# Optimization experiments

Hardware: AMD Instinct MI355X
Metric: run time of the kernel (lower is better)

Reference implementation:

```python
import jax, jax.numpy as jnp
import numpy as np

V, D, N, M, H, W, K = 97, 512, 128, 64, 8, 8, 3
HALF = K // 2
DH = D // H
RPL = M + 3 + K   # key(M) + beta + gate + shift(K) + gamma = 70
WPL = RPL + 2 * M # + erase(M) + add(M) = 198
B, T = 32, 128


def _ln(x, g, b):
    mu = x.mean(-1, keepdims=True)
    var = ((x - mu) ** 2).mean(-1, keepdims=True)
    return (x - mu) / jnp.sqrt(var + 1e-5) * g + b


def _addressing(key, beta, gate, shift, gamma, prev_w, memory):
    # key [B,M], beta/gate/gamma [B,1], shift [B,K], prev_w [B,N], memory [B,N,M]
    eps = 1e-12
    kn = key / (jnp.linalg.norm(key, axis=-1, keepdims=True) + eps)
    mn = memory / (jnp.linalg.norm(memory, axis=-1, keepdims=True) + eps)
    cos = jnp.einsum('bnm,bm->bn', mn, kn)
    wc = jax.nn.softmax(jax.nn.softplus(beta) * cos, axis=-1)
    g = jax.nn.sigmoid(gate)
    wg = g * wc + (1.0 - g) * prev_w
    s = jax.nn.softmax(shift, axis=-1)
    shifted = sum(s[:, k:k + 1] * jnp.roll(wg, k - HALF, axis=-1) for k in range(K))
    gp = 1.0 + jax.nn.softplus(gamma)
    wt = (shifted + eps) ** gp
    return wt / (wt.sum(-1, keepdims=True) + eps)


def setup_inputs() -> dict:
    key = jax.random.key(0)
    ks = jax.random.split(key, 16)
    s = 0.05
    return {
        'x': jax.random.randint(ks[0], (B, T), 0, V),
        'emb': jax.random.normal(ks[1], (V, D)) * 0.02,
        'W_in': jax.random.normal(ks[2], (D, D + M)) * s,
        'b_in': jnp.zeros((D,)),
        'W_qkv': jax.random.normal(ks[3], (3 * D, D)) * s,
        'b_qkv': jnp.zeros((3 * D,)),
        'W_o': jax.random.normal(ks[4], (D, D)) * s,
        'b_o': jnp.zeros((D,)),
        'ln1_g': jnp.ones((D,)), 'ln1_b': jnp.zeros((D,)),
        'W_ff1': jax.random.normal(ks[5], (4 * D, D)) * s,
        'b_ff1': jnp.zeros((4 * D,)),
        'W_ff2': jax.random.normal(ks[6], (D, 4 * D)) * s,
        'b_ff2': jnp.zeros((D,)),
        'ln2_g': jnp.ones((D,)), 'ln2_b': jnp.zeros((D,)),
        'W_tok': jax.random.normal(ks[7], (V, D)) * s,
        'b_tok': jnp.zeros((V,)),
        'W_read': jax.random.normal(ks[8], (RPL, D)) * s,
        'b_read': jnp.zeros((RPL,)),
        'W_write': jax.random.normal(ks[9], (WPL, D)) * s,
        'b_write': jnp.zeros((WPL,)),
    }


def _forward(x, emb, W_in, b_in, W_qkv, b_qkv, W_o, b_o, ln1_g, ln1_b,
             W_ff1, b_ff1, W_ff2, b_ff2, ln2_g, ln2_b, W_tok, b_tok,
             W_read, b_read, W_write, b_write):
    Wq, Wk, Wv = W_qkv[:D], W_qkv[D:2 * D], W_qkv[2 * D:]
    bq, bk, bv = b_qkv[:D], b_qkv[D:2 * D], b_qkv[2 * D:]
    scale = 1.0 / np.sqrt(DH)

    def step(carry, x_t):
        memory, rw, ww, cache, t = carry
        tok = emb[x_t]                                   # [B,D]
        r = jnp.einsum('bn,bnm->bm', rw, memory)         # read vector [B,M]
        wide = jnp.concatenate([tok, r], -1)             # [B,D+M]
        xp = wide @ W_in.T + b_in                        # [B,D]
        q = xp[None]                                     # [1,B,D]
        # kv buffer: cache (detached) + current q, truncated to last W
        kbuf = jnp.concatenate([cache, q], 0)[-W:]       # [W,B,D]
        valid = jnp.arange(W) >= W - jnp.minimum(t + 1, W)
        qh = (xp @ Wq.T + bq).reshape(-1, H, DH)         # [B,H,DH]
        kh = (kbuf @ Wk.T + bk).reshape(W, -1, H, DH)    # [W,B,H,DH]
        vh = (kbuf @ Wv.T + bv).reshape(W, -1, H, DH)
        scores = jnp.einsum('bhe,wbhe->bhw', qh, kh) * scale
        scores = jnp.where(valid[None, None, :], scores, -jnp.inf)
        attn = jax.nn.softmax(scores, axis=-1)
        ctx = jnp.einsum('bhw,wbhe->bhe', attn, vh).reshape(-1, D)
        attn_out = ctx @ W_o.T + b_o
        x2 = _ln(xp + attn_out, ln1_g, ln1_b)
        ff = jax.nn.gelu(x2 @ W_ff1.T + b_ff1, approximate=False) @ W_ff2.T + b_ff2
        out = _ln(x2 + ff, ln2_g, ln2_b)
        logits = out @ W_tok.T + b_tok
        # read head addressing (RH=1)
        rp = out @ W_read.T + b_read
        new_rw = _addressing(rp[:, :M], rp[:, M:M + 1], rp[:, M + 1:M + 2],
                             rp[:, M + 2:M + 2 + K], rp[:, M + 2 + K:M + 3 + K],
                             rw, memory)
        # write head addressing + erase/add (WH=1)
        wp = out @ W_write.T + b_write
        new_ww = _addressing(wp[:, :M], wp[:, M:M + 1], wp[:, M + 1:M + 2],
                             wp[:, M + 2:M + 2 + K], wp[:, M + 2 + K:M + 3 + K],
                             ww, memory)
        erase = jax.nn.sigmoid(wp[:, RPL:RPL + M])       # [B,M]
        add = jnp.tanh(wp[:, RPL + M:])                  # [B,M]
        new_mem = memory * (1.0 - new_ww[:, :, None] * erase[:, None, :]) \
                  + new_ww[:, :, None] * add[:, None, :]
        new_cache = jax.lax.stop_gradient(jnp.concatenate([cache, q], 0)[-W:])
        return (new_mem, new_rw, new_ww, new_cache, t + 1), logits

    Bv = x.shape[0]
    mem0 = jnp.zeros((Bv, N, M), jnp.float32)
    w0 = jnp.zeros((Bv, N), jnp.float32).at[:, 0].set(1.0)
    cache0 = jnp.zeros((W, Bv, D), jnp.float32)
    carry0 = (mem0, w0, w0, cache0, jnp.int32(0))
    _, logits = jax.lax.scan(step, carry0, x.T)          # [T,B,V]
    return jnp.transpose(logits, (1, 0, 2))              # [B,T,V]


def reference(x, emb, W_in, b_in, W_qkv, b_qkv, W_o, b_o, ln1_g, ln1_b,
              W_ff1, b_ff1, W_ff2, b_ff2, ln2_g, ln2_b, W_tok, b_tok,
              W_read, b_read, W_write, b_write):
    return _forward(x, emb, W_in, b_in, W_qkv, b_qkv, W_o, b_o, ln1_g, ln1_b,
                    W_ff1, b_ff1, W_ff2, b_ff2, ln2_g, ln2_b, W_tok, b_tok,
                    W_read, b_read, W_write, b_write)
```

## Files before the change

kernel.cpp:

```cpp
#include <hip/hip_runtime.h>
#include <math.h>

static constexpr int Tc = 128, Vc = 97;

static constexpr size_t T_FQ  = 0;
static constexpr size_t BF    = T_FQ + (size_t)576*1536;
static constexpr size_t T_IN  = BF + 1536;
static constexpr size_t T_O   = T_IN + (size_t)576*512;
static constexpr size_t T_FF1 = T_O + (size_t)512*512;
static constexpr size_t T_FF2 = T_FF1 + (size_t)512*2048;
static constexpr size_t T_TOK = T_FF2 + (size_t)2048*512;
static constexpr size_t T_RW  = T_TOK + (size_t)512*128;
static constexpr size_t ARENA = T_RW + (size_t)512*288;
static constexpr size_t TEAM_STRIDE = 8704;
static constexpr size_t A_YP = 0;
static constexpr size_t A_OP = 4096;
static constexpr size_t A_RWP = 8192;
static constexpr size_t FLG = ARENA + (size_t)32*TEAM_STRIDE;

__device__ __forceinline__ float softplusf_(float x) { return x > 20.f ? x : log1pf(expf(x)); }
__device__ __forceinline__ float sigmoidf_(float x) { return 1.f / (1.f + expf(-x)); }

__device__ __forceinline__ float wsum(float v) {
#pragma unroll
  for (int o = 1; o < 64; o <<= 1) v += __shfl_xor(v, o);
  return v;
}
__device__ __forceinline__ float wmax(float v) {
#pragma unroll
  for (int o = 1; o < 64; o <<= 1) v = fmaxf(v, __shfl_xor(v, o));
  return v;
}

__device__ __forceinline__ void st_llc(float* p, float v) {
  __hip_atomic_store(p, v, __ATOMIC_RELAXED, __HIP_MEMORY_SCOPE_SYSTEM);
}
__device__ __forceinline__ float ld_llc(const float* p) {
  return __hip_atomic_load(p, __ATOMIC_RELAXED, __HIP_MEMORY_SCOPE_SYSTEM);
}
__device__ __forceinline__ void st_flag(int* p, int v) {
  __hip_atomic_store(p, v, __ATOMIC_RELAXED, __HIP_MEMORY_SCOPE_SYSTEM);
}
__device__ __forceinline__ int ld_flag(const int* p) {
  return __hip_atomic_load(p, __ATOMIC_RELAXED, __HIP_MEMORY_SCOPE_SYSTEM);
}

#define PUBF(stage)                                                      \
  do {                                                                   \
    asm volatile("s_waitcnt vmcnt(0)" ::: "memory");                     \
    __syncthreads();                                                     \
    if (tid == 0) st_flag(flg + (stage)*128 + sq*16, t + 1);             \
  } while (0)

#define WAITF(stage, need)                                               \
  do {                                                                   \
    if (tid < 8) {                                                       \
      while (ld_flag(flg + (stage)*128 + tid*16) < (need))               \
        __builtin_amdgcn_s_sleep(1);                                     \
    }                                                                    \
    __syncthreads();                                                     \
    asm volatile("" ::: "memory");                                       \
  } while (0)

template <int NCH, int CH, int NG, int SF4>
__device__ __forceinline__ void mvp(const float* __restrict__ wbase,
                                    const float* __restrict__ src,
                                    float* part, int tid) {
  const int cs = tid / NG, g = tid % NG;
  const float4* __restrict__ w4 =
      reinterpret_cast<const float4*>(wbase + (size_t)cs * CH * (SF4 * 4)) + g;
  const float* __restrict__ v = src + cs * CH;
  float a0 = 0.f, a1 = 0.f, a2 = 0.f, a3 = 0.f;
#pragma unroll 8
  for (int c = 0; c < CH; ++c) {
    float4 w = w4[(size_t)c * SF4];
    float vv = v[c];
    a0 += vv * w.x; a1 += vv * w.y; a2 += vv * w.z; a3 += vv * w.w;
  }
  *reinterpret_cast<float4*>(part + tid * 4) = make_float4(a0, a1, a2, a3);
}

__global__ __launch_bounds__(256) void k_init(const float* __restrict__ W_in,
                                              const float* __restrict__ W_qkv,
                                              const float* __restrict__ W_o,
                                              const float* __restrict__ W_ff1,
                                              const float* __restrict__ W_ff2,
                                              const float* __restrict__ W_tok,
                                              const float* __restrict__ W_read,
                                              const float* __restrict__ W_write,
                                              const float* __restrict__ b_qkv,
                                              const float* __restrict__ b_in,
                                              float* __restrict__ ws) {
  const size_t tid = (size_t)blockIdx.x * 256 + threadIdx.x;
  const size_t nth = (size_t)gridDim.x * 256;
  for (size_t i = tid; i < (size_t)576*512; i += nth) {
    size_t c = i >> 9, j = i & 511;
    ws[T_IN + i] = W_in[j * 576 + c];
  }
  for (size_t i = tid; i < (size_t)512*512; i += nth) {
    size_t e = i >> 9, j = i & 511;
    ws[T_O + i] = W_o[j * 512 + e];
  }
  for (size_t i = tid; i < (size_t)512*2048; i += nth) {
    size_t d = i >> 11, f = i & 2047;
    ws[T_FF1 + i] = W_ff1[f * 512 + d];
  }
  for (size_t i = tid; i < (size_t)2048*512; i += nth) {
    size_t k = i >> 9, j = i & 511;
    ws[T_FF2 + i] = W_ff2[j * 2048 + k];
  }
  for (size_t i = tid; i < (size_t)512*128; i += nth) {
    size_t d = i >> 7, j = i & 127;
    int qq = (int)(j >> 4), i2 = (int)(j & 15);
    int v = qq * 13 + i2;
    ws[T_TOK + i] = (i2 < 13 && v < 97) ? W_tok[(size_t)v * 512 + d] : 0.f;
  }
  for (size_t i = tid; i < (size_t)512*288; i += nth) {
    size_t d = i / 288, j = i % 288;
    int qq = (int)(j / 36), i2 = (int)(j % 36);
    int idx = qq * 34 + i2;
    float val = 0.f;
    if (i2 < 34 && idx < 268)
      val = (idx < 70) ? W_read[(size_t)idx * 512 + d] : W_write[(size_t)(idx - 70) * 512 + d];
    ws[T_RW + i] = val;
  }
  for (size_t j = tid; j < 1536; j += nth) {
    float a = b_qkv[j];
    const float* r = W_qkv + j * 512;
    for (int d = 0; d < 512; ++d) a += r[d] * b_in[d];
    ws[BF + j] = a;
  }
  for (size_t i = tid; i < (size_t)32 * TEAM_STRIDE; i += nth) ws[ARENA + i] = 0.f;
  for (size_t i = tid; i < 32768; i += nth) ((int*)(ws + FLG))[i] = 0;
}

__global__ __launch_bounds__(256) void k_fuse(const float* __restrict__ W_qkv,
                                              const float* __restrict__ W_in,
                                              float* __restrict__ ws) {
  __shared__ float As[32][64];
  __shared__ float Bs[32][96];
  const int cb = blockIdx.x % 9, jb = blockIdx.x / 9;
  const int c0 = cb * 64, j0 = jb * 96;
  const int tid = threadIdx.x;
  float acc[24];
#pragma unroll
  for (int u = 0; u < 24; ++u) acc[u] = 0.f;
  for (int d0 = 0; d0 < 512; d0 += 32) {
    __syncthreads();
    for (int i = tid; i < 32 * 64; i += 256) { int dd = i >> 6, cc = i & 63; As[dd][cc] = W_in[(size_t)(d0 + dd) * 576 + c0 + cc]; }
    for (int i = tid; i < 32 * 96; i += 256) { int jj = i >> 5, dd = i & 31; Bs[dd][jj] = W_qkv[(size_t)(j0 + jj) * 512 + d0 + dd]; }
    __syncthreads();
    const int tc = tid & 63, jbase = (tid >> 6) * 24;
    for (int dd = 0; dd < 32; ++dd) {
      float a = As[dd][tc];
#pragma unroll
      for (int u = 0; u < 24; ++u) acc[u] += a * Bs[dd][jbase + u];
    }
  }
  const int tc = tid & 63, jbase = (tid >> 6) * 24;
#pragma unroll
  for (int u = 0; u < 24; ++u)
    ws[T_FQ + (size_t)(c0 + tc) * 1536 + j0 + jbase + u] = acc[u];
}

__global__ __launch_bounds__(512) void k_main(
    const int* __restrict__ x, const float* __restrict__ emb,
    const float* __restrict__ b_in, const float* __restrict__ b_o,
    const float* __restrict__ ln1g, const float* __restrict__ ln1b,
    const float* __restrict__ b_ff1, const float* __restrict__ b_ff2,
    const float* __restrict__ ln2g, const float* __restrict__ ln2b,
    const float* __restrict__ b_tok,
    const float* __restrict__ b_read, const float* __restrict__ b_write,
    float* __restrict__ ws, float* __restrict__ dout) {
  const float* __restrict__ wt = ws;
  const int wg = blockIdx.x, tid = threadIdx.x;
  const int sq = wg & 7, b = wg >> 3;
  const int wv = tid >> 6, ln = tid & 63;
  float* ar = ws + ARENA + (size_t)b * TEAM_STRIDE;
  int* flg = (int*)(ws + FLG) + b * 1024;

  __shared__ float memS[128 * 64];
  __shared__ float kcS[8 * 64], vcS[8 * 64];
  __shared__ float rwvS[128], wwvS[128], wwnS[128];
  __shared__ float rvec[64];
  __shared__ float wideS[576];
  __shared__ float xpSl[64];
  __shared__ float qhS[64];
  __shared__ float scoresS[8], awS[8];
  __shared__ float ctxH[64];
  __shared__ float yS[512], x2S[512], oS[512], onS[512];
  __shared__ float hSl[256];
  __shared__ __align__(16) float part[2048];
  __shared__ float rwpS[272];
  __shared__ float cosS[256];
  __shared__ float redA[8], redB[8];
  __shared__ float eS[64], aS[64];

  for (int i = tid; i < 8192; i += 512) memS[i] = 0.f;
  if (tid < 128) { float v0 = (tid == 0) ? 1.f : 0.f; rwvS[tid] = v0; wwvS[tid] = v0; }
  __syncthreads();

  for (int t = 0; t < Tc; ++t) {
    {
      float a = 0.f;
#pragma unroll
      for (int k2 = 0; k2 < 16; ++k2) { int n = wv * 16 + k2; a += rwvS[n] * memS[n * 64 + ln]; }
      part[wv * 64 + ln] = a;
    }
    __syncthreads();
    if (tid < 64) {
      float s = 0.f;
#pragma unroll
      for (int p = 0; p < 8; ++p) s += part[p * 64 + tid];
      rvec[tid] = s;
    }
    __syncthreads();
    const int tok = x[b * Tc + t];
    for (int i = tid; i < 576; i += 512)
      wideS[i] = (i < 512) ? emb[(size_t)tok * 512 + i] : rvec[i - 512];
    __syncthreads();

    const int slot = t & 7;
    for (int p3 = 0; p3 < 3; ++p3) {
      mvp<32, 18, 16, 384>(wt + T_FQ + p3 * 512 + 64 * sq, wideS, part, tid);
      __syncthreads();
      if (tid < 64) {
        float s = wt[BF + p3 * 512 + 64 * sq + tid];
#pragma unroll
        for (int cs = 0; cs < 32; ++cs) s += part[cs * 64 + tid];
        if (p3 == 0) qhS[tid] = s;
        else if (p3 == 1) kcS[slot * 64 + tid] = s;
        else vcS[slot * 64 + tid] = s;
      }
      __syncthreads();
    }
    mvp<32, 18, 16, 128>(wt + T_IN + 64 * sq, wideS, part, tid);
    __syncthreads();
    if (tid < 64) {
      float s = b_in[64 * sq + tid];
#pragma unroll
      for (int cs = 0; cs < 32; ++cs) s += part[cs * 64 + tid];
      xpSl[tid] = s;
    }
    __syncthreads();

    {
      int st = t - 7 + wv;
      float c = 0.f;
      if (st >= 0) c = qhS[ln] * kcS[(st & 7) * 64 + ln];
      c = wsum(c);
      if (ln == 0) scoresS[wv] = (st >= 0) ? c * 0.125f : -INFINITY;
    }
    __syncthreads();
    if (tid == 0) {
      float mx = -INFINITY;
      for (int j = 0; j < 8; ++j) mx = fmaxf(mx, scoresS[j]);
      float e[8], ssum = 0.f;
      for (int j = 0; j < 8; ++j) { e[j] = expf(scoresS[j] - mx); ssum += e[j]; }
      float inv = 1.f / ssum;
      for (int j = 0; j < 8; ++j) awS[j] = e[j] * inv;
    }
    __syncthreads();
    if (tid < 64) {
      float a = 0.f;
#pragma unroll
      for (int j = 0; j < 8; ++j) {
        int st = t - 7 + j;
        if (st >= 0) a += awS[j] * vcS[(st & 7) * 64 + tid];
      }
      ctxH[tid] = a;
    }
    __syncthreads();

    mvp<4, 16, 128, 128>(wt + T_O + (size_t)64 * sq * 512, ctxH, part, tid);
    __syncthreads();
    {
      float s = 0.f;
#pragma unroll
      for (int cs = 0; cs < 4; ++cs) s += part[cs * 512 + tid];
      if ((tid >> 6) == sq) s += xpSl[tid & 63];
      st_llc(ar + A_YP + sq * 512 + tid, s);
    }
    PUBF(0);
    WAITF(0, t + 1);
    {
      float s = b_o[tid];
#pragma unroll
      for (int q2 = 0; q2 < 8; ++q2) s += ld_llc(ar + A_YP + q2 * 512 + tid);
      yS[tid] = s;
    }
    __syncthreads();
    {
      float v = yS[tid];
      float a = wsum(v), b2 = wsum(v * v);
      if (ln == 0) { redA[wv] = a; redB[wv] = b2; }
      __syncthreads();
      float sa = 0.f, sb = 0.f;
#pragma unroll
      for (int i2 = 0; i2 < 8; ++i2) { sa += redA[i2]; sb += redB[i2]; }
      float mu = sa * (1.f / 512.f);
      float var = sb * (1.f / 512.f) - mu * mu;
      float rstd = rsqrtf(var + 1e-5f);
      x2S[tid] = (yS[tid] - mu) * rstd * ln1g[tid] + ln1b[tid];
    }
    __syncthreads();

    mvp<8, 64, 64, 512>(wt + T_FF1 + 256 * sq, x2S, part, tid);
    __syncthreads();
    if (tid < 256) {
      float s = b_ff1[256 * sq + tid];
#pragma unroll
      for (int cs = 0; cs < 8; ++cs) s += part[cs * 256 + tid];
      hSl[tid] = 0.5f * s * (1.f + erff(s * 0.70710678118654752f));
    }
    __syncthreads();

    mvp<4, 64, 128, 128>(wt + T_FF2 + (size_t)256 * sq * 512, hSl, part, tid);
    __syncthreads();
    {
      float s = 0.f;
#pragma unroll
      for (int cs = 0; cs < 4; ++cs) s += part[cs * 512 + tid];
      st_llc(ar + A_OP + sq * 512 + tid, s);
    }
    PUBF(1);
    WAITF(1, t + 1);
    {
      float s = b_ff2[tid] + x2S[tid];
#pragma unroll
      for (int q2 = 0; q2 < 8; ++q2) s += ld_llc(ar + A_OP + q2 * 512 + tid);
      oS[tid] = s;
    }
    __syncthreads();
    {
      float v = oS[tid];
      float a = wsum(v), b2 = wsum(v * v);
      if (ln == 0) { redA[wv] = a; redB[wv] = b2; }
      __syncthreads();
      float sa = 0.f, sb = 0.f;
#pragma unroll
      for (int i2 = 0; i2 < 8; ++i2) { sa += redA[i2]; sb += redB[i2]; }
      float mu = sa * (1.f / 512.f);
      float var = sb * (1.f / 512.f) - mu * mu;
      float rstd = rsqrtf(var + 1e-5f);
      onS[tid] = (oS[tid] - mu) * rstd * ln2g[tid] + ln2b[tid];
    }
    __syncthreads();

    if (tid < 288) {
      const int cs = tid / 9, g = tid % 9;
      const float4* __restrict__ w4 =
          reinterpret_cast<const float4*>(wt + T_RW + (size_t)(cs * 16) * 288 + 36 * sq) + g;
      const float* __restrict__ v = onS + cs * 16;
      float a0 = 0.f, a1 = 0.f, a2 = 0.f, a3 = 0.f;
#pragma unroll
      for (int c = 0; c < 16; ++c) {
        float4 w = w4[(size_t)c * 72];
        float vv = v[c];
        a0 += vv * w.x; a1 += vv * w.y; a2 += vv * w.z; a3 += vv * w.w;
      }
      *reinterpret_cast<float4*>(part + cs * 36 + g * 4) = make_float4(a0, a1, a2, a3);
    }
    __syncthreads();
    if (tid < 34) {
      int idx = 34 * sq + tid;
      if (idx < 268) {
        float s = (idx < 70) ? b_read[idx] : b_write[idx - 70];
#pragma unroll
        for (int cs = 0; cs < 32; ++cs) s += part[cs * 36 + tid];
        st_llc(ar + A_RWP + idx, s);
      }
    }
    PUBF(2);
    if (tid < 128) {
      const int cs = tid >> 2, g = tid & 3;
      const float4* __restrict__ w4 =
          reinterpret_cast<const float4*>(wt + T_TOK + (size_t)(cs * 16) * 128 + 16 * sq) + g;
      const float* __restrict__ v = onS + cs * 16;
      float a0 = 0.f, a1 = 0.f, a2 = 0.f, a3 = 0.f;
#pragma unroll
      for (int c = 0; c < 16; ++c) {
        float4 w = w4[(size_t)c * 32];
        float vv = v[c];
        a0 += vv * w.x; a1 += vv * w.y; a2 += vv * w.z; a3 += vv * w.w;
      }
      *reinterpret_cast<float4*>(part + tid * 4) = make_float4(a0, a1, a2, a3);
    }
    __syncthreads();
    if (tid < 13) {
      int v = 13 * sq + tid;
      if (v < Vc) {
        float s = b_tok[v];
#pragma unroll
        for (int cs = 0; cs < 32; ++cs) s += part[cs * 16 + tid];
        dout[((size_t)b * Tc + t) * Vc + v] = s;
      }
    }
    WAITF(2, t + 1);
    if (tid < 268) rwpS[tid] = ld_llc(ar + A_RWP + tid);
    __syncthreads();

    for (int p = 0; p < 32; ++p) {
      int idx = wv * 32 + p;
      int ksel = idx >> 7, row = idx & 127;
      const float* key = ksel ? (rwpS + 70) : rwpS;
      float m = memS[row * 64 + ln];
      float pp = m * key[ln], qq = m * m;
#pragma unroll
      for (int o = 1; o < 64; o <<= 1) { pp += __shfl_xor(pp, o); qq += __shfl_xor(qq, o); }
      if (ln == 0) cosS[idx] = pp / (sqrtf(qq) + 1e-12f);
    }
    __syncthreads();
    if (wv < 2) {
      const float* P = wv ? (rwpS + 70) : rwpS;
      const float* cosb = cosS + wv * 128;
      float* prevw = wv ? wwvS : rwvS;
      float kk = P[ln];
      float kn2 = wsum(kk * kk);
      float kinv = 1.f / (sqrtf(kn2) + 1e-12f);
      float beta = softplusf_(P[64]);
      float g = sigmoidf_(P[65]);
      float sh0 = P[66], sh1 = P[67], sh2 = P[68];
      float m3 = fmaxf(sh0, fmaxf(sh1, sh2));
      float es0 = expf(sh0 - m3), es1 = expf(sh1 - m3), es2 = expf(sh2 - m3);
      float i3 = 1.f / (es0 + es1 + es2);
      es0 *= i3; es1 *= i3; es2 *= i3;
      float gp = 1.f + softplusf_(P[69]);
      float v0 = beta * cosb[ln] * kinv, v1 = beta * cosb[64 + ln] * kinv;
      float mx = wmax(fmaxf(v0, v1));
      float e0 = expf(v0 - mx), e1 = expf(v1 - mx);
      float einv = 1.f / wsum(e0 + e1);
      float w0 = g * e0 * einv + (1.f - g) * prevw[ln];
      float w1 = g * e1 * einv + (1.f - g) * prevw[64 + ln];
      float w0m = __shfl(w0, (ln + 63) & 63), w1m = __shfl(w1, (ln + 63) & 63);
      float w0p = __shfl(w0, (ln + 1) & 63),  w1p = __shfl(w1, (ln + 1) & 63);
      float prev0 = (ln == 0)  ? w1m : w0m;
      float next0 = (ln == 63) ? w1p : w0p;
      float prev1 = (ln == 0)  ? w0m : w1m;
      float next1 = (ln == 63) ? w0p : w1p;
      float t0 = es0 * next0 + es1 * w0 + es2 * prev0;
      float t1 = es0 * next1 + es1 * w1 + es2 * prev1;
      float wt0 = powf(t0 + 1e-12f, gp), wt1 = powf(t1 + 1e-12f, gp);
      float winv = 1.f / (wsum(wt0 + wt1) + 1e-12f);
      w0 = wt0 * winv; w1 = wt1 * winv;
      prevw[ln] = w0; prevw[64 + ln] = w1;
      if (wv) { wwnS[ln] = w0; wwnS[64 + ln] = w1; }
    } else if (wv == 2) {
      eS[ln] = sigmoidf_(rwpS[140 + ln]);
      aS[ln] = tanhf(rwpS[204 + ln]);
    }
    __syncthreads();
    for (int i = tid; i < 8192; i += 512) {
      int n = i >> 6, m = i & 63;
      float wn = wwnS[n];
      memS[i] = memS[i] * (1.f - wn * eS[m]) + wn * aS[m];
    }
    __syncthreads();
  }
}

extern "C" void kernel_launch(void* const* d_in, const int* in_sizes, int n_in,
                              void* d_out, int out_size, void* d_ws, size_t ws_size,
                              hipStream_t stream) {
  (void)in_sizes; (void)n_in; (void)out_size; (void)ws_size;
  const int* x = (const int*)d_in[0];
  const float* emb = (const float*)d_in[1];
  const float* W_in = (const float*)d_in[2];
  const float* b_in = (const float*)d_in[3];
  const float* W_qkv = (const float*)d_in[4];
  const float* b_qkv = (const float*)d_in[5];
  const float* W_o = (const float*)d_in[6];
  const float* b_o = (const float*)d_in[7];
  const float* ln1g = (const float*)d_in[8];
  const float* ln1b = (const float*)d_in[9];
  const float* W_ff1 = (const float*)d_in[10];
  const float* b_ff1 = (const float*)d_in[11];
  const float* W_ff2 = (const float*)d_in[12];
  const float* b_ff2 = (const float*)d_in[13];
  const float* ln2g = (const float*)d_in[14];
  const float* ln2b = (const float*)d_in[15];
  const float* W_tok = (const float*)d_in[16];
  const float* b_tok = (const float*)d_in[17];
  const float* W_read = (const float*)d_in[18];
  const float* b_read = (const float*)d_in[19];
  const float* W_write = (const float*)d_in[20];
  const float* b_write = (const float*)d_in[21];
  float* ws = (float*)d_ws;
  float* out = (float*)d_out;

  hipLaunchKernelGGL(k_init, dim3(512), dim3(256), 0, stream,
                     W_in, W_qkv, W_o, W_ff1, W_ff2, W_tok, W_read, W_write,
                     b_qkv, b_in, ws);
  hipLaunchKernelGGL(k_fuse, dim3(144), dim3(256), 0, stream, W_qkv, W_in, ws);
  hipLaunchKernelGGL(k_main, dim3(256), dim3(512), 0, stream,
                     x, emb, b_in, b_o, ln1g, ln1b, b_ff1, b_ff2,
                     ln2g, ln2b, b_tok, b_read, b_write, ws, out);
}
```

Before: 6.163 ms.

## Repartition persistent kernel by output columns across whole batch with global stage flags

The persistent kernel no longer has each batch row handled by a team of 8 workgroups. Each workgroup now computes a column slice of every projection (QKV/in, O, FF1, FF2, read/write, token logits) for all 32 batch rows, so each weight slice is loaded once into LDS and reused across the batch. Stages are chained through global flags and atomic stores. Memory addressing stays on 32 workgroups, which now also keep the memory row norms incrementally. The change trades heavy per-team weight streaming for more grid-wide synchronization points per timestep (about six global barriers per step).

```diff
diff --git a/kernel.cpp b/kernel.cpp
--- a/kernel.cpp
+++ b/kernel.cpp
@@ -3,20 +3,24 @@
 
 static constexpr int Tc = 128, Vc = 97;
 
-static constexpr size_t T_FQ  = 0;
-static constexpr size_t BF    = T_FQ + (size_t)576*1536;
-static constexpr size_t T_IN  = BF + 1536;
-static constexpr size_t T_O   = T_IN + (size_t)576*512;
-static constexpr size_t T_FF1 = T_O + (size_t)512*512;
-static constexpr size_t T_FF2 = T_FF1 + (size_t)512*2048;
-static constexpr size_t T_TOK = T_FF2 + (size_t)2048*512;
-static constexpr size_t T_RW  = T_TOK + (size_t)512*128;
-static constexpr size_t ARENA = T_RW + (size_t)512*288;
-static constexpr size_t TEAM_STRIDE = 8704;
-static constexpr size_t A_YP = 0;
-static constexpr size_t A_OP = 4096;
-static constexpr size_t A_RWP = 8192;
-static constexpr size_t FLG = ARENA + (size_t)32*TEAM_STRIDE;
+static constexpr size_t T_FQ = 0;
+static constexpr size_t BF   = T_FQ + (size_t)576*1536;
+static constexpr size_t T_IN = BF + 1536;
+static constexpr size_t T_O  = T_IN + (size_t)576*512;
+static constexpr size_t T_FF1= T_O + (size_t)512*512;
+static constexpr size_t T_FF2= T_FF1 + (size_t)512*2048;
+static constexpr size_t T_RW = T_FF2 + (size_t)2048*512;
+static constexpr size_t A_WIDE = T_RW + (size_t)512*272;
+static constexpr size_t A_QKVX = A_WIDE + (size_t)32*576;
+static constexpr size_t A_CTX  = A_QKVX + (size_t)4*32*512;
+static constexpr size_t A_Y    = A_CTX + (size_t)32*512;
+static constexpr size_t A_H    = A_Y + (size_t)32*512;
+static constexpr size_t A_OUT  = A_H + (size_t)32*2048;
+static constexpr size_t A_X2   = A_OUT + (size_t)32*512;
+static constexpr size_t A_RWP  = A_X2 + (size_t)32*512;
+static constexpr size_t FLGO   = A_RWP + (size_t)32*272;
+static constexpr int FA_S=0, FB_S=256, FC1_S=512, FC2_S=768, FD_S=1024, FE1_S=1280, FE2_S=1536;
+static constexpr int NFLG_INT = 1792 * 16;
 
 __device__ __forceinline__ float softplusf_(float x) { return x > 20.f ? x : log1pf(expf(x)); }
 __device__ __forceinline__ float sigmoidf_(float x) { return 1.f / (1.f + expf(-x)); }
@@ -35,61 +39,34 @@
 __device__ __forceinline__ void st_llc(float* p, float v) {
   __hip_atomic_store(p, v, __ATOMIC_RELAXED, __HIP_MEMORY_SCOPE_SYSTEM);
 }
-__device__ __forceinline__ float ld_llc(const float* p) {
-  return __hip_atomic_load(p, __ATOMIC_RELAXED, __HIP_MEMORY_SCOPE_SYSTEM);
-}
 __device__ __forceinline__ void st_flag(int* p, int v) {
   __hip_atomic_store(p, v, __ATOMIC_RELAXED, __HIP_MEMORY_SCOPE_SYSTEM);
 }
 __device__ __forceinline__ int ld_flag(const int* p) {
   return __hip_atomic_load(p, __ATOMIC_RELAXED, __HIP_MEMORY_SCOPE_SYSTEM);
 }
-
-#define PUBF(stage)                                                      \
-  do {                                                                   \
-    asm volatile("s_waitcnt vmcnt(0)" ::: "memory");                     \
-    __syncthreads();                                                     \
-    if (tid == 0) st_flag(flg + (stage)*128 + sq*16, t + 1);             \
+__device__ __forceinline__ void wait1(const int* flg, int slot, int need) {
+  while (ld_flag(flg + slot * 16) < need) __builtin_amdgcn_s_sleep(1);
+}
+#define FENCE_ACQ() __builtin_amdgcn_fence(__ATOMIC_ACQUIRE, "agent")
+#define PUBF(slot)                                            \
+  do {                                                        \
+    asm volatile("s_waitcnt vmcnt(0)" ::: "memory");          \
+    __syncthreads();                                          \
+    if (tid == 0) st_flag(flg + (slot) * 16, t + 1);          \
   } while (0)
 
-#define WAITF(stage, need)                                               \
-  do {                                                                   \
-    if (tid < 8) {                                                       \
-      while (ld_flag(flg + (stage)*128 + tid*16) < (need))               \
-        __builtin_amdgcn_s_sleep(1);                                     \
-    }                                                                    \
-    __syncthreads();                                                     \
-    asm volatile("" ::: "memory");                                       \
-  } while (0)
-
-template <int NCH, int CH, int NG, int SF4>
-__device__ __forceinline__ void mvp(const float* __restrict__ wbase,
-                                    const float* __restrict__ src,
-                                    float* part, int tid) {
-  const int cs = tid / NG, g = tid % NG;
-  const float4* __restrict__ w4 =
-      reinterpret_cast<const float4*>(wbase + (size_t)cs * CH * (SF4 * 4)) + g;
-  const float* __restrict__ v = src + cs * CH;
-  float a0 = 0.f, a1 = 0.f, a2 = 0.f, a3 = 0.f;
-#pragma unroll 8
-  for (int c = 0; c < CH; ++c) {
-    float4 w = w4[(size_t)c * SF4];
-    float vv = v[c];
-    a0 += vv * w.x; a1 += vv * w.y; a2 += vv * w.z; a3 += vv * w.w;
-  }
-  *reinterpret_cast<float4*>(part + tid * 4) = make_float4(a0, a1, a2, a3);
-}
-
 __global__ __launch_bounds__(256) void k_init(const float* __restrict__ W_in,
-                                              const float* __restrict__ W_qkv,
                                               const float* __restrict__ W_o,
                                               const float* __restrict__ W_ff1,
                                               const float* __restrict__ W_ff2,
-                                              const float* __restrict__ W_tok,
                                               const float* __restrict__ W_read,
                                               const float* __restrict__ W_write,
+                                              const float* __restrict__ W_qkv,
                                               const float* __restrict__ b_qkv,
                                               const float* __restrict__ b_in,
+                                              const float* __restrict__ emb,
+                                              const int* __restrict__ x,
                                               float* __restrict__ ws) {
   const size_t tid = (size_t)blockIdx.x * 256 + threadIdx.x;
   const size_t nth = (size_t)gridDim.x * 256;
@@ -109,20 +86,12 @@
     size_t k = i >> 9, j = i & 511;
     ws[T_FF2 + i] = W_ff2[j * 2048 + k];
   }
-  for (size_t i = tid; i < (size_t)512*128; i += nth) {
-    size_t d = i >> 7, j = i & 127;
-    int qq = (int)(j >> 4), i2 = (int)(j & 15);
-    int v = qq * 13 + i2;
-    ws[T_TOK + i] = (i2 < 13 && v < 97) ? W_tok[(size_t)v * 512 + d] : 0.f;
-  }
-  for (size_t i = tid; i < (size_t)512*288; i += nth) {
-    size_t d = i / 288, j = i % 288;
-    int qq = (int)(j / 36), i2 = (int)(j % 36);
-    int idx = qq * 34 + i2;
-    float val = 0.f;
-    if (i2 < 34 && idx < 268)
-      val = (idx < 70) ? W_read[(size_t)idx * 512 + d] : W_write[(size_t)(idx - 70) * 512 + d];
-    ws[T_RW + i] = val;
+  for (size_t i = tid; i < (size_t)512*272; i += nth) {
+    size_t d = i / 272, j = i % 272;
+    float v = 0.f;
+    if (j < 70) v = W_read[j * 512 + d];
+    else if (j < 268) v = W_write[(j - 70) * 512 + d];
+    ws[T_RW + i] = v;
   }
   for (size_t j = tid; j < 1536; j += nth) {
     float a = b_qkv[j];
@@ -130,8 +99,11 @@
     for (int d = 0; d < 512; ++d) a += r[d] * b_in[d];
     ws[BF + j] = a;
   }
-  for (size_t i = tid; i < (size_t)32 * TEAM_STRIDE; i += nth) ws[ARENA + i] = 0.f;
-  for (size_t i = tid; i < 32768; i += nth) ((int*)(ws + FLG))[i] = 0;
+  for (size_t i = tid; i < (size_t)32*576; i += nth) {
+    size_t b = i / 576, c = i % 576;
+    ws[A_WIDE + i] = (c < 512) ? emb[(size_t)x[b * 128] * 512 + c] : 0.f;
+  }
+  for (size_t i = tid; i < (size_t)NFLG_INT; i += nth) ((int*)(ws + FLGO))[i] = 0;
 }
 
 __global__ __launch_bounds__(256) void k_fuse(const float* __restrict__ W_qkv,
@@ -169,293 +141,405 @@
     const float* __restrict__ ln1g, const float* __restrict__ ln1b,
     const float* __restrict__ b_ff1, const float* __restrict__ b_ff2,
     const float* __restrict__ ln2g, const float* __restrict__ ln2b,
-    const float* __restrict__ b_tok,
+    const float* __restrict__ W_tok, const float* __restrict__ b_tok,
     const float* __restrict__ b_read, const float* __restrict__ b_write,
     float* __restrict__ ws, float* __restrict__ dout) {
   const float* __restrict__ wt = ws;
-  const int wg = blockIdx.x, tid = threadIdx.x;
-  const int sq = wg & 7, b = wg >> 3;
-  const int wv = tid >> 6, ln = tid & 63;
-  float* ar = ws + ARENA + (size_t)b * TEAM_STRIDE;
-  int* flg = (int*)(ws + FLG) + b * 1024;
+  const int g = blockIdx.x, tid = threadIdx.x;
+  const int b = tid >> 4, u = tid & 15;
+  const int ln = tid & 63, wv = tid >> 6;
+  int* flg = (int*)(ws + FLGO);
 
   __shared__ float memS[128 * 64];
+  __shared__ float ssq[128];
   __shared__ float kcS[8 * 64], vcS[8 * 64];
   __shared__ float rwvS[128], wwvS[128], wwnS[128];
-  __shared__ float rvec[64];
-  __shared__ float wideS[576];
-  __shared__ float xpSl[64];
-  __shared__ float qhS[64];
-  __shared__ float scoresS[8], awS[8];
-  __shared__ float ctxH[64];
-  __shared__ float yS[512], x2S[512], oS[512], onS[512];
-  __shared__ float hSl[256];
-  __shared__ __align__(16) float part[2048];
+  __shared__ float xbuf[32 * 512];
+  __shared__ float wS[4608];
+  __shared__ float pbuf[4096];
   __shared__ float rwpS[272];
-  __shared__ float cosS[256];
-  __shared__ float redA[8], redB[8];
+  __shared__ float cosR[128], cosW[128];
   __shared__ float eS[64], aS[64];
-
+  __shared__ float muS[32], rsS[32];
+  __shared__ float qS[64], scoresS[8], awS[8], rvec[64];
+
+  if (tid < 128) {
+    ssq[tid] = 0.f;
+    float v0 = (tid == 0) ? 1.f : 0.f;
+    rwvS[tid] = v0; wwvS[tid] = v0;
+  }
   for (int i = tid; i < 8192; i += 512) memS[i] = 0.f;
-  if (tid < 128) { float v0 = (tid == 0) ? 1.f : 0.f; rwvS[tid] = v0; wwvS[tid] = v0; }
   __syncthreads();
 
+  const int partA = g >> 6, subA = g & 63, jcA = subA * 8;
+  const int bB = g >> 3, hB = g & 7;
+
   for (int t = 0; t < Tc; ++t) {
+    if (tid < 32) wait1(flg, FE2_S + tid, t);
+    __syncthreads();
+    FENCE_ACQ();
     {
-      float a = 0.f;
-#pragma unroll
-      for (int k2 = 0; k2 < 16; ++k2) { int n = wv * 16 + k2; a += rwvS[n] * memS[n * 64 + ln]; }
-      part[wv * 64 + ln] = a;
-    }
-    __syncthreads();
-    if (tid < 64) {
-      float s = 0.f;
-#pragma unroll
-      for (int p = 0; p < 8; ++p) s += part[p * 64 + tid];
-      rvec[tid] = s;
-    }
-    __syncthreads();
-    const int tok = x[b * Tc + t];
-    for (int i = tid; i < 576; i += 512)
-      wideS[i] = (i < 512) ? emb[(size_t)tok * 512 + i] : rvec[i - 512];
-    __syncthreads();
-
-    const int slot = t & 7;
-    for (int p3 = 0; p3 < 3; ++p3) {
-      mvp<32, 18, 16, 384>(wt + T_FQ + p3 * 512 + 64 * sq, wideS, part, tid);
+      const size_t wbase = (partA < 3) ? (T_FQ + (size_t)partA * 512 + jcA) : (T_IN + jcA);
+      const size_t wstr = (partA < 3) ? 1536 : 512;
+      for (int i = tid; i < 4608; i += 512) {
+        int d = i >> 3, u8 = i & 7;
+        wS[i] = wt[wbase + (size_t)d * wstr + u8];
+      }
+      __syncthreads();
+      float acc[8];
+#pragma unroll
+      for (int i = 0; i < 8; ++i) acc[i] = 0.f;
+      const float* wrow = ws + A_WIDE + b * 576 + u * 36;
+      for (int dd = 0; dd < 36; ++dd) {
+        float wv2 = wrow[dd];
+        const float* wl = wS + (u * 36 + dd) * 8;
+#pragma unroll
+        for (int i = 0; i < 8; ++i) acc[i] += wv2 * wl[i];
+      }
+      float* pp = pbuf + tid * 8;
+#pragma unroll
+      for (int i = 0; i < 8; ++i) pp[i] = acc[i];
+      __syncthreads();
+      if (u < 8) {
+        float s = (partA < 3) ? wt[BF + partA * 512 + jcA + u] : b_in[jcA + u];
+        for (int k = 0; k < 16; ++k) s += pbuf[(b * 16 + k) * 8 + u];
+        st_llc(ws + A_QKVX + ((size_t)partA * 32 + b) * 512 + jcA + u, s);
+      }
+    }
+    PUBF(FA_S + g);
+
+    if (tid < 24) { int pt = tid >> 3, uu = tid & 7; wait1(flg, FA_S + pt * 64 + 8 * hB + uu, t + 1); }
+    __syncthreads();
+    FENCE_ACQ();
+    {
+      const int slot = t & 7;
+      if (tid < 64) qS[tid] = ws[A_QKVX + (size_t)(0 * 32 + bB) * 512 + 64 * hB + tid];
+      else if (tid < 128) kcS[slot * 64 + tid - 64] = ws[A_QKVX + (size_t)(32 + bB) * 512 + 64 * hB + tid - 64];
+      else if (tid < 192) vcS[slot * 64 + tid - 128] = ws[A_QKVX + (size_t)(64 + bB) * 512 + 64 * hB + tid - 128];
+      __syncthreads();
+      {
+        int st = t - 7 + wv;
+        float c = (st >= 0) ? qS[ln] * kcS[(st & 7) * 64 + ln] : 0.f;
+        c = wsum(c);
+        if (ln == 0) scoresS[wv] = (st >= 0) ? c * 0.125f : -INFINITY;
+      }
+      __syncthreads();
+      if (tid == 0) {
+        float mx = -INFINITY;
+        for (int j = 0; j < 8; ++j) mx = fmaxf(mx, scoresS[j]);
+        float e[8], ssm = 0.f;
+        for (int j = 0; j < 8; ++j) { e[j] = expf(scoresS[j] - mx); ssm += e[j]; }
+        float inv = 1.f / ssm;
+        for (int j = 0; j < 8; ++j) awS[j] = e[j] * inv;
+      }
       __syncthreads();
       if (tid < 64) {
-        float s = wt[BF + p3 * 512 + 64 * sq + tid];
-#pragma unroll
-        for (int cs = 0; cs < 32; ++cs) s += part[cs * 64 + tid];
-        if (p3 == 0) qhS[tid] = s;
-        else if (p3 == 1) kcS[slot * 64 + tid] = s;
-        else vcS[slot * 64 + tid] = s;
-      }
-      __syncthreads();
-    }
-    mvp<32, 18, 16, 128>(wt + T_IN + 64 * sq, wideS, part, tid);
-    __syncthreads();
-    if (tid < 64) {
-      float s = b_in[64 * sq + tid];
-#pragma unroll
-      for (int cs = 0; cs < 32; ++cs) s += part[cs * 64 + tid];
-      xpSl[tid] = s;
-    }
-    __syncthreads();
-
+        float a = 0.f;
+#pragma unroll
+        for (int j = 0; j < 8; ++j) {
+          int st = t - 7 + j;
+          if (st >= 0) a += awS[j] * vcS[(st & 7) * 64 + tid];
+        }
+        st_llc(ws + A_CTX + (size_t)bB * 512 + 64 * hB + tid, a);
+      }
+    }
+    PUBF(FB_S + g);
+
+    if (tid < 256) wait1(flg, FB_S + tid, t + 1);
+    else if (tid < 320) wait1(flg, FA_S + 192 + (tid - 256), t + 1);
+    __syncthreads();
+    FENCE_ACQ();
     {
-      int st = t - 7 + wv;
-      float c = 0.f;
-      if (st >= 0) c = qhS[ln] * kcS[(st & 7) * 64 + ln];
-      c = wsum(c);
-      if (ln == 0) scoresS[wv] = (st >= 0) ? c * 0.125f : -INFINITY;
-    }
-    __syncthreads();
-    if (tid == 0) {
-      float mx = -INFINITY;
-      for (int j = 0; j < 8; ++j) mx = fmaxf(mx, scoresS[j]);
-      float e[8], ssum = 0.f;
-      for (int j = 0; j < 8; ++j) { e[j] = expf(scoresS[j] - mx); ssum += e[j]; }
-      float inv = 1.f / ssum;
-      for (int j = 0; j < 8; ++j) awS[j] = e[j] * inv;
-    }
-    __syncthreads();
-    if (tid < 64) {
-      float a = 0.f;
-#pragma unroll
-      for (int j = 0; j < 8; ++j) {
-        int st = t - 7 + j;
-        if (st >= 0) a += awS[j] * vcS[(st & 7) * 64 + tid];
-      }
-      ctxH[tid] = a;
-    }
-    __syncthreads();
-
-    mvp<4, 16, 128, 128>(wt + T_O + (size_t)64 * sq * 512, ctxH, part, tid);
-    __syncthreads();
+      for (int i = tid; i < 1024; i += 512) {
+        int e = i >> 1, c = i & 1;
+        wS[i] = wt[T_O + (size_t)e * 512 + 2 * g + c];
+      }
+      __syncthreads();
+      float a0 = 0.f, a1 = 0.f;
+      const float* crow = ws + A_CTX + (size_t)b * 512 + u * 32;
+#pragma unroll
+      for (int dd = 0; dd < 32; ++dd) {
+        float cv = crow[dd];
+        a0 += cv * wS[(u * 32 + dd) * 2];
+        a1 += cv * wS[(u * 32 + dd) * 2 + 1];
+      }
+      pbuf[tid * 2] = a0; pbuf[tid * 2 + 1] = a1;
+      __syncthreads();
+      if (u < 2) {
+        float s = b_o[2 * g + u] + ws[A_QKVX + (size_t)(96 + b) * 512 + 2 * g + u];
+        for (int k = 0; k < 16; ++k) s += pbuf[(b * 16 + k) * 2 + u];
+        st_llc(ws + A_Y + (size_t)b * 512 + 2 * g + u, s);
+      }
+    }
+    PUBF(FC1_S + g);
+
+    if (tid < 256) wait1(flg, FC1_S + tid, t + 1);
+    __syncthreads();
+    FENCE_ACQ();
     {
-      float s = 0.f;
-#pragma unroll
-      for (int cs = 0; cs < 4; ++cs) s += part[cs * 512 + tid];
-      if ((tid >> 6) == sq) s += xpSl[tid & 63];
-      st_llc(ar + A_YP + sq * 512 + tid, s);
-    }
-    PUBF(0);
-    WAITF(0, t + 1);
+      float yv[32];
+      float s1 = 0.f, s2 = 0.f;
+      const float* yrow = ws + A_Y + (size_t)b * 512 + u * 32;
+#pragma unroll
+      for (int dd = 0; dd < 32; ++dd) { yv[dd] = yrow[dd]; s1 += yv[dd]; s2 += yv[dd] * yv[dd]; }
+      pbuf[tid] = s1; pbuf[512 + tid] = s2;
+      __syncthreads();
+      if (u == 0) {
+        float sa = 0.f, sb = 0.f;
+        for (int k = 0; k < 16; ++k) { sa += pbuf[b * 16 + k]; sb += pbuf[512 + b * 16 + k]; }
+        float mu = sa * (1.f / 512.f);
+        float var = sb * (1.f / 512.f) - mu * mu;
+        muS[b] = mu; rsS[b] = rsqrtf(var + 1e-5f);
+      }
+      __syncthreads();
+      {
+        float mu = muS[b], rs = rsS[b];
+#pragma unroll
+        for (int dd = 0; dd < 32; ++dd) {
+          int d = u * 32 + dd;
+          xbuf[b * 512 + d] = (yv[dd] - mu) * rs * ln1g[d] + ln1b[d];
+        }
+      }
+      __syncthreads();
+      for (int i = tid; i < 4096; i += 512) {
+        int d = i >> 3, u8 = i & 7;
+        wS[i] = wt[T_FF1 + (size_t)d * 2048 + 8 * g + u8];
+      }
+      __syncthreads();
+      float acc[8];
+#pragma unroll
+      for (int i = 0; i < 8; ++i) acc[i] = 0.f;
+#pragma unroll
+      for (int dd = 0; dd < 32; ++dd) {
+        float xv = xbuf[b * 512 + u * 32 + dd];
+        const float* wl = wS + (u * 32 + dd) * 8;
+#pragma unroll
+        for (int i = 0; i < 8; ++i) acc[i] += xv * wl[i];
+      }
+      float* pp = pbuf + tid * 8;
+#pragma unroll
+      for (int i = 0; i < 8; ++i) pp[i] = acc[i];
+      __syncthreads();
+      if (u < 8) {
+        float s = b_ff1[8 * g + u];
+        for (int k = 0; k < 16; ++k) s += pbuf[(b * 16 + k) * 8 + u];
+        st_llc(ws + A_H + (size_t)b * 2048 + 8 * g + u, 0.5f * s * (1.f + erff(s * 0.70710678118654752f)));
+      } else if (u < 10) {
+        st_llc(ws + A_X2 + (size_t)b * 512 + 2 * g + (u - 8), xbuf[b * 512 + 2 * g + (u - 8)]);
+      }
+    }
+    PUBF(FC2_S + g);
+
+    if (tid < 256) wait1(flg, FC2_S + tid, t + 1);
+    __syncthreads();
+    FENCE_ACQ();
     {
-      float s = b_o[tid];
-#pragma unroll
-      for (int q2 = 0; q2 < 8; ++q2) s += ld_llc(ar + A_YP + q2 * 512 + tid);
-      yS[tid] = s;
-    }
-    __syncthreads();
-    {
-      float v = yS[tid];
-      float a = wsum(v), b2 = wsum(v * v);
-      if (ln == 0) { redA[wv] = a; redB[wv] = b2; }
-      __syncthreads();
-      float sa = 0.f, sb = 0.f;
-#pragma unroll
-      for (int i2 = 0; i2 < 8; ++i2) { sa += redA[i2]; sb += redB[i2]; }
-      float mu = sa * (1.f / 512.f);
-      float var = sb * (1.f / 512.f) - mu * mu;
-      float rstd = rsqrtf(var + 1e-5f);
-      x2S[tid] = (yS[tid] - mu) * rstd * ln1g[tid] + ln1b[tid];
-    }
-    __syncthreads();
-
-    mvp<8, 64, 64, 512>(wt + T_FF1 + 256 * sq, x2S, part, tid);
-    __syncthreads();
-    if (tid < 256) {
-      float s = b_ff1[256 * sq + tid];
-#pragma unroll
-      for (int cs = 0; cs < 8; ++cs) s += part[cs * 256 + tid];
-      hSl[tid] = 0.5f * s * (1.f + erff(s * 0.70710678118654752f));
-    }
-    __syncthreads();
-
-    mvp<4, 64, 128, 128>(wt + T_FF2 + (size_t)256 * sq * 512, hSl, part, tid);
-    __syncthreads();
-    {
-      float s = 0.f;
-#pragma unroll
-      for (int cs = 0; cs < 4; ++cs) s += part[cs * 512 + tid];
-      st_llc(ar + A_OP + sq * 512 + tid, s);
-    }
-    PUBF(1);
-    WAITF(1, t + 1);
-    {
-      float s = b_ff2[tid] + x2S[tid];
-#pragma unroll
-      for (int q2 = 0; q2 < 8; ++q2) s += ld_llc(ar + A_OP + q2 * 512 + tid);
-      oS[tid] = s;
-    }
-    __syncthreads();
-    {
-      float v = oS[tid];
-      float a = wsum(v), b2 = wsum(v * v);
-      if (ln == 0) { redA[wv] = a; redB[wv] = b2; }
-      __syncthreads();
-      float sa = 0.f, sb = 0.f;
-#pragma unroll
-      for (int i2 = 0; i2 < 8; ++i2) { sa += redA[i2]; sb += redB[i2]; }
-      float mu = sa * (1.f / 512.f);
-      float var = sb * (1.f / 512.f) - mu * mu;
-      float rstd = rsqrtf(var + 1e-5f);
-      onS[tid] = (oS[tid] - mu) * rstd * ln2g[tid] + ln2b[tid];
-    }
-    __syncthreads();
-
-    if (tid < 288) {
-      const int cs = tid / 9, g = tid % 9;
-      const float4* __restrict__ w4 =
-          reinterpret_cast<const float4*>(wt + T_RW + (size_t)(cs * 16) * 288 + 36 * sq) + g;
-      const float* __restrict__ v = onS + cs * 16;
-      float a0 = 0.f, a1 = 0.f, a2 = 0.f, a3 = 0.f;
-#pragma unroll
-      for (int c = 0; c < 16; ++c) {
-        float4 w = w4[(size_t)c * 72];
-        float vv = v[c];
-        a0 += vv * w.x; a1 += vv * w.y; a2 += vv * w.z; a3 += vv * w.w;
-      }
-      *reinterpret_cast<float4*>(part + cs * 36 + g * 4) = make_float4(a0, a1, a2, a3);
-    }
-    __syncthreads();
-    if (tid < 34) {
-      int idx = 34 * sq + tid;
-      if (idx < 268) {
-        float s = (idx < 70) ? b_read[idx] : b_write[idx - 70];
-#pragma unroll
-        for (int cs = 0; cs < 32; ++cs) s += part[cs * 36 + tid];
-        st_llc(ar + A_RWP + idx, s);
-      }
-    }
-    PUBF(2);
-    if (tid < 128) {
-      const int cs = tid >> 2, g = tid & 3;
-      const float4* __restrict__ w4 =
-          reinterpret_cast<const float4*>(wt + T_TOK + (size_t)(cs * 16) * 128 + 16 * sq) + g;
-      const float* __restrict__ v = onS + cs * 16;
-      float a0 = 0.f, a1 = 0.f, a2 = 0.f, a3 = 0.f;
-#pragma unroll
-      for (int c = 0; c < 16; ++c) {
-        float4 w = w4[(size_t)c * 32];
-        float vv = v[c];
-        a0 += vv * w.x; a1 += vv * w.y; a2 += vv * w.z; a3 += vv * w.w;
-      }
-      *reinterpret_cast<float4*>(part + tid * 4) = make_float4(a0, a1, a2, a3);
-    }
-    __syncthreads();
-    if (tid < 13) {
-      int v = 13 * sq + tid;
-      if (v < Vc) {
-        float s = b_tok[v];
-#pragma unroll
-        for (int cs = 0; cs < 32; ++cs) s += part[cs * 16 + tid];
-        dout[((size_t)b * Tc + t) * Vc + v] = s;
-      }
-    }
-    WAITF(2, t + 1);
-    if (tid < 268) rwpS[tid] = ld_llc(ar + A_RWP + tid);
-    __syncthreads();
-
-    for (int p = 0; p < 32; ++p) {
-      int idx = wv * 32 + p;
-      int ksel = idx >> 7, row = idx & 127;
-      const float* key = ksel ? (rwpS + 70) : rwpS;
-      float m = memS[row * 64 + ln];
-      float pp = m * key[ln], qq = m * m;
-#pragma unroll
-      for (int o = 1; o < 64; o <<= 1) { pp += __shfl_xor(pp, o); qq += __shfl_xor(qq, o); }
-      if (ln == 0) cosS[idx] = pp / (sqrtf(qq) + 1e-12f);
-    }
-    __syncthreads();
-    if (wv < 2) {
-      const float* P = wv ? (rwpS + 70) : rwpS;
-      const float* cosb = cosS + wv * 128;
-      float* prevw = wv ? wwvS : rwvS;
-      float kk = P[ln];
-      float kn2 = wsum(kk * kk);
-      float kinv = 1.f / (sqrtf(kn2) + 1e-12f);
-      float beta = softplusf_(P[64]);
-      float g = sigmoidf_(P[65]);
-      float sh0 = P[66], sh1 = P[67], sh2 = P[68];
-      float m3 = fmaxf(sh0, fmaxf(sh1, sh2));
-      float es0 = expf(sh0 - m3), es1 = expf(sh1 - m3), es2 = expf(sh2 - m3);
-      float i3 = 1.f / (es0 + es1 + es2);
-      es0 *= i3; es1 *= i3; es2 *= i3;
-      float gp = 1.f + softplusf_(P[69]);
-      float v0 = beta * cosb[ln] * kinv, v1 = beta * cosb[64 + ln] * kinv;
-      float mx = wmax(fmaxf(v0, v1));
-      float e0 = expf(v0 - mx), e1 = expf(v1 - mx);
-      float einv = 1.f / wsum(e0 + e1);
-      float w0 = g * e0 * einv + (1.f - g) * prevw[ln];
-      float w1 = g * e1 * einv + (1.f - g) * prevw[64 + ln];
-      float w0m = __shfl(w0, (ln + 63) & 63), w1m = __shfl(w1, (ln + 63) & 63);
-      float w0p = __shfl(w0, (ln + 1) & 63),  w1p = __shfl(w1, (ln + 1) & 63);
-      float prev0 = (ln == 0)  ? w1m : w0m;
-      float next0 = (ln == 63) ? w1p : w0p;
-      float prev1 = (ln == 0)  ? w0m : w1m;
-      float next1 = (ln == 63) ? w0p : w1p;
-      float t0 = es0 * next0 + es1 * w0 + es2 * prev0;
-      float t1 = es0 * next1 + es1 * w1 + es2 * prev1;
-      float wt0 = powf(t0 + 1e-12f, gp), wt1 = powf(t1 + 1e-12f, gp);
-      float winv = 1.f / (wsum(wt0 + wt1) + 1e-12f);
-      w0 = wt0 * winv; w1 = wt1 * winv;
-      prevw[ln] = w0; prevw[64 + ln] = w1;
-      if (wv) { wwnS[ln] = w0; wwnS[64 + ln] = w1; }
-    } else if (wv == 2) {
-      eS[ln] = sigmoidf_(rwpS[140 + ln]);
-      aS[ln] = tanhf(rwpS[204 + ln]);
-    }
-    __syncthreads();
-    for (int i = tid; i < 8192; i += 512) {
-      int n = i >> 6, m = i & 63;
-      float wn = wwnS[n];
-      memS[i] = memS[i] * (1.f - wn * eS[m]) + wn * aS[m];
-    }
-    __syncthreads();
+      for (int i = tid; i < 4096; i += 512) {
+        int k = i >> 1, c = i & 1;
+        wS[i] = wt[T_FF2 + (size_t)k * 512 + 2 * g + c];
+      }
+      __syncthreads();
+      float a0 = 0.f, a1 = 0.f;
+      const float4* hrow = reinterpret_cast<const float4*>(ws + A_H + (size_t)b * 2048 + u * 128);
+#pragma unroll 8
+      for (int q4 = 0; q4 < 32; ++q4) {
+        float4 hv = hrow[q4];
+        const float* wl = wS + (u * 128 + q4 * 4) * 2;
+        a0 += hv.x * wl[0] + hv.y * wl[2] + hv.z * wl[4] + hv.w * wl[6];
+        a1 += hv.x * wl[1] + hv.y * wl[3] + hv.z * wl[5] + hv.w * wl[7];
+      }
+      pbuf[tid * 2] = a0; pbuf[tid * 2 + 1] = a1;
+      __syncthreads();
+      if (u < 2) {
+        float s = b_ff2[2 * g + u] + ws[A_X2 + (size_t)b * 512 + 2 * g + u];
+        for (int k = 0; k < 16; ++k) s += pbuf[(b * 16 + k) * 2 + u];
+        st_llc(ws + A_OUT + (size_t)b * 512 + 2 * g + u, s);
+      }
+    }
+    PUBF(FD_S + g);
+
+    if (tid < 256) wait1(flg, FD_S + tid, t + 1);
+    __syncthreads();
+    FENCE_ACQ();
+    if (g < 231) {
+      float ov[32];
+      float s1 = 0.f, s2 = 0.f;
+      const float* orow = ws + A_OUT + (size_t)b * 512 + u * 32;
+#pragma unroll
+      for (int dd = 0; dd < 32; ++dd) { ov[dd] = orow[dd]; s1 += ov[dd]; s2 += ov[dd] * ov[dd]; }
+      pbuf[tid] = s1; pbuf[512 + tid] = s2;
+      __syncthreads();
+      if (u == 0) {
+        float sa = 0.f, sb = 0.f;
+        for (int k = 0; k < 16; ++k) { sa += pbuf[b * 16 + k]; sb += pbuf[512 + b * 16 + k]; }
+        float mu = sa * (1.f / 512.f);
+        float var = sb * (1.f / 512.f) - mu * mu;
+        muS[b] = mu; rsS[b] = rsqrtf(var + 1e-5f);
+      }
+      __syncthreads();
+      {
+        float mu = muS[b], rs = rsS[b];
+#pragma unroll
+        for (int dd = 0; dd < 32; ++dd) {
+          int d = u * 32 + dd;
+          xbuf[b * 512 + d] = (ov[dd] - mu) * rs * ln2g[d] + ln2b[d];
+        }
+      }
+      __syncthreads();
+      if (g < 134) {
+        for (int i = tid; i < 1024; i += 512) {
+          int d = i >> 1, c = i & 1;
+          wS[i] = wt[T_RW + (size_t)d * 272 + 2 * g + c];
+        }
+        __syncthreads();
+        float a0 = 0.f, a1 = 0.f;
+#pragma unroll
+        for (int dd = 0; dd < 32; ++dd) {
+          float xv = xbuf[b * 512 + u * 32 + dd];
+          a0 += xv * wS[(u * 32 + dd) * 2];
+          a1 += xv * wS[(u * 32 + dd) * 2 + 1];
+        }
+        pbuf[tid * 2] = a0; pbuf[tid * 2 + 1] = a1;
+        __syncthreads();
+        if (u < 2) {
+          int c = 2 * g + u;
+          float s = (c < 70) ? b_read[c] : b_write[c - 70];
+          for (int k = 0; k < 16; ++k) s += pbuf[(b * 16 + k) * 2 + u];
+          st_llc(ws + A_RWP + (size_t)b * 272 + c, s);
+        }
+      } else {
+        const int v = g - 134;
+        if (tid < 512) wS[tid] = W_tok[(size_t)v * 512 + tid];
+        __syncthreads();
+        float a0 = 0.f;
+#pragma unroll
+        for (int dd = 0; dd < 32; ++dd) a0 += xbuf[b * 512 + u * 32 + dd] * wS[u * 32 + dd];
+        pbuf[tid] = a0;
+        __syncthreads();
+        if (u == 0) {
+          float s = b_tok[v];
+          for (int k = 0; k < 16; ++k) s += pbuf[b * 16 + k];
+          dout[((size_t)b * Tc + t) * Vc + v] = s;
+        }
+      }
+    }
+    PUBF(FE1_S + g);
+
+    if (g < 32 && t < Tc - 1) {
+      if (tid < 134) wait1(flg, FE1_S + tid, t + 1);
+      __syncthreads();
+      FENCE_ACQ();
+      if (tid < 268) rwpS[tid] = ws[A_RWP + (size_t)g * 272 + tid];
+      __syncthreads();
+      {
+        const int n = tid >> 2, gg = tid & 3;
+        float pR = 0.f, pW = 0.f;
+#pragma unroll
+        for (int dd = 0; dd < 16; ++dd) {
+          int e = gg * 16 + dd;
+          float m = memS[n * 64 + e];
+          pR += m * rwpS[e];
+          pW += m * rwpS[70 + e];
+        }
+        pbuf[tid] = pR; pbuf[2048 + tid] = pW;
+        __syncthreads();
+        if (gg == 0) {
+          float dR = 0.f, dW = 0.f;
+#pragma unroll
+          for (int k = 0; k < 4; ++k) { dR += pbuf[n * 4 + k]; dW += pbuf[2048 + n * 4 + k]; }
+          float den = sqrtf(ssq[n]) + 1e-12f;
+          cosR[n] = dR / den;
+          cosW[n] = dW / den;
+        }
+      }
+      __syncthreads();
+      if (wv < 2) {
+        const float* P = wv ? (rwpS + 70) : rwpS;
+        const float* cosb = wv ? cosW : cosR;
+        float* prevw = wv ? wwvS : rwvS;
+        float kk = P[ln];
+        float kn2 = wsum(kk * kk);
+        float kinv = 1.f / (sqrtf(kn2) + 1e-12f);
+        float beta = softplusf_(P[64]);
+        float gg2 = sigmoidf_(P[65]);
+        float sh0 = P[66], sh1 = P[67], sh2 = P[68];
+        float m3 = fmaxf(sh0, fmaxf(sh1, sh2));
+        float es0 = expf(sh0 - m3), es1 = expf(sh1 - m3), es2 = expf(sh2 - m3);
+        float i3 = 1.f / (es0 + es1 + es2);
+        es0 *= i3; es1 *= i3; es2 *= i3;
+        float gp = 1.f + softplusf_(P[69]);
+        float v0 = beta * cosb[ln] * kinv, v1 = beta * cosb[64 + ln] * kinv;
+        float mx = wmax(fmaxf(v0, v1));
+        float e0 = expf(v0 - mx), e1 = expf(v1 - mx);
+        float einv = 1.f / wsum(e0 + e1);
+        float w0 = gg2 * e0 * einv + (1.f - gg2) * prevw[ln];
+        float w1 = gg2 * e1 * einv + (1.f - gg2) * prevw[64 + ln];
+        float w0m = __shfl(w0, (ln + 63) & 63), w1m = __shfl(w1, (ln + 63) & 63);
+        float w0p = __shfl(w0, (ln + 1) & 63), w1p = __shfl(w1, (ln + 1) & 63);
+        float prev0 = (ln == 0) ? w1m : w0m;
+        float next0 = (ln == 63) ? w1p : w0p;
+        float prev1 = (ln == 0) ? w0m : w1m;
+        float next1 = (ln == 63) ? w0p : w1p;
+        float t0 = es0 * next0 + es1 * w0 + es2 * prev0;
+        float t1 = es0 * next1 + es1 * w1 + es2 * prev1;
+        float wt0 = powf(t0 + 1e-12f, gp), wt1 = powf(t1 + 1e-12f, gp);
+        float winv = 1.f / (wsum(wt0 + wt1) + 1e-12f);
+        w0 = wt0 * winv; w1 = wt1 * winv;
+        prevw[ln] = w0; prevw[64 + ln] = w1;
+        if (wv) { wwnS[ln] = w0; wwnS[64 + ln] = w1; }
+      } else if (wv == 2) {
+        eS[ln] = sigmoidf_(rwpS[140 + ln]);
+        aS[ln] = tanhf(rwpS[204 + ln]);
+      }
+      __syncthreads();
+      {
+        const int n = tid >> 2, gg = tid & 3;
+        float wn = wwnS[n];
+        float sq = 0.f;
+#pragma unroll
+        for (int dd = 0; dd < 16; ++dd) {
+          int m = gg * 16 + dd;
+          float v = memS[n * 64 + m] * (1.f - wn * eS[m]) + wn * aS[m];
+          memS[n * 64 + m] = v;
+          sq += v * v;
+        }
+        pbuf[tid] = sq;
+        __syncthreads();
+        if (gg == 0) {
+          float s = 0.f;
+#pragma unroll
+          for (int k = 0; k < 4; ++k) s += pbuf[n * 4 + k];
+          ssq[n] = s;
+        }
+      }
+      __syncthreads();
+      {
+        const int ee = tid & 63, ng = tid >> 6;
+        float s = 0.f;
+#pragma unroll
+        for (int k = 0; k < 16; ++k) {
+          int n = ng * 16 + k;
+          s += rwvS[n] * memS[n * 64 + ee];
+        }
+        pbuf[ng * 64 + ee] = s;
+      }
+      __syncthreads();
+      if (tid < 64) {
+        float s = 0.f;
+#pragma unroll
+        for (int k = 0; k < 8; ++k) s += pbuf[k * 64 + tid];
+        rvec[tid] = s;
+      }
+      __syncthreads();
+      {
+        const int tok2 = x[g * Tc + t + 1];
+        for (int i = tid; i < 576; i += 512) {
+          float v = (i < 512) ? emb[(size_t)tok2 * 512 + i] : rvec[i - 512];
+          st_llc(ws + A_WIDE + (size_t)g * 576 + i, v);
+        }
+      }
+      PUBF(FE2_S + g);
+    }
   }
 }
 
@@ -489,10 +573,9 @@
   float* out = (float*)d_out;
 
   hipLaunchKernelGGL(k_init, dim3(512), dim3(256), 0, stream,
-                     W_in, W_qkv, W_o, W_ff1, W_ff2, W_tok, W_read, W_write,
-                     b_qkv, b_in, ws);
+                     W_in, W_o, W_ff1, W_ff2, W_read, W_write, W_qkv, b_qkv, b_in, emb, x, ws);
   hipLaunchKernelGGL(k_fuse, dim3(144), dim3(256), 0, stream, W_qkv, W_in, ws);
   hipLaunchKernelGGL(k_main, dim3(256), dim3(512), 0, stream,
                      x, emb, b_in, b_o, ln1g, ln1b, b_ff1, b_ff2,
-                     ln2g, ln2b, b_tok, b_read, b_write, ws, out);
-}
+                     ln2g, ln2b, W_tok, b_tok, b_read, b_write, ws, out);
+}
```

Result: slower. 23.77 ms (+285.8%).
